# Performance work log

Measured on AMD Instinct MI355X. Metric: run time of the kernel, lower is better.

Reference implementation:

```python
import jax, jax.numpy as jnp
import numpy as np

N = 50000   # nnodes
E = 1600000 # edges (avg degree 32)
F = 128     # nfeatures
D = 64      # output_dim
T = 10      # s2v iterations (default in n2v)


def setup_inputs() -> dict:
    key = jax.random.key(0)
    k_x, k_s, k_d, k_w1, k_w2 = jax.random.split(key, 5)
    x = jax.random.normal(k_x, (N, F), dtype=jnp.float32)
    edge_src = jax.random.randint(k_s, (E,), 0, N, dtype=jnp.int32)
    edge_dst = jax.random.randint(k_d, (E,), 0, N, dtype=jnp.int32)
    # xavier_uniform init as in reset_parameters
    s1 = float(np.sqrt(6.0 / (F + D)))
    s2 = float(np.sqrt(6.0 / (D + D)))
    W1 = jax.random.uniform(k_w1, (D, F), jnp.float32, -s1, s1)
    W2 = jax.random.uniform(k_w2, (D, D), jnp.float32, -s2, s2)
    b1 = jnp.zeros((D,), jnp.float32)
    b2 = jnp.zeros((D,), jnp.float32)
    return {"x": x, "W1": W1, "b1": b1, "W2": W2, "b2": b2,
            "edge_src": edge_src, "edge_dst": edge_dst}


def reference(x, W1, b1, W2, b2, edge_src, edge_dst):
    Wx = x @ W1.T + b1                      # [N, D]

    def step(emb, _):
        # sum of neighbor embeddings: gather sources, segment-sum into dests
        agg = jax.ops.segment_sum(emb[edge_src], edge_dst, num_segments=N)  # [N, D]
        emb_new = jax.nn.relu(Wx + agg @ W2.T + b2)
        return emb_new, None

    emb0 = jnp.zeros((N, D), dtype=x.dtype)
    emb, _ = jax.lax.scan(step, emb0, None, length=T)  # n2v
    # g2v: sum node embeddings into graph embedding
    return emb.sum(axis=0)                  # [D]
```

## Files before the change

### kernel.cpp

```cpp
#include <hip/hip_runtime.h>

#define D 64
#define F 128
#define NBMAX 256
#define DB 128

typedef unsigned int uint;
typedef unsigned short ushort;
typedef short s16x8 __attribute__((ext_vector_type(8)));
typedef float f32x4 __attribute__((ext_vector_type(4)));

__device__ __forceinline__ float bf16lo(uint u) { return __uint_as_float(u << 16); }
__device__ __forceinline__ float bf16hi(uint u) { return __uint_as_float(u & 0xFFFF0000u); }
__device__ __forceinline__ ushort f2bf16(float f) {
    uint u = __float_as_uint(f);
    u += 0x7FFFu + ((u >> 16) & 1u);
    return (ushort)(u >> 16);
}
__device__ __forceinline__ uint pk2bf(float lo, float hi) {
    return (uint)f2bf16(lo) | ((uint)f2bf16(hi) << 16);
}


__global__ __launch_bounds__(256) void bucket_hist(const int* __restrict__ dst,
                                                   int* __restrict__ gb, int E, int nb) {
    __shared__ int h[NBMAX];
    for (int t = threadIdx.x; t < nb; t += 256) h[t] = 0;
    __syncthreads();
    int start = blockIdx.x * 4096;
    int end   = start + 4096 < E ? start + 4096 : E;
    for (int i = start + threadIdx.x; i < end; i += 256)
        atomicAdd(&h[dst[i] >> 8], 1);
    __syncthreads();
    for (int t = threadIdx.x; t < nb; t += 256)
        if (h[t]) atomicAdd(&gb[t], h[t]);
}

__global__ void bucket_scan(const int* __restrict__ gb, int* __restrict__ gboff,
                            int* __restrict__ gcur, int nb) {
    if (threadIdx.x == 0) {
        int s = 0;
        for (int b = 0; b < nb; ++b) { gboff[b] = s; gcur[b] = s; s += gb[b]; }
        gboff[nb] = s;
    }
}

__global__ __launch_bounds__(256) void bucket_scatter(const int* __restrict__ src,
                                                      const int* __restrict__ dst,
                                                      int* __restrict__ gcur,
                                                      int* __restrict__ packed, int E, int nb) {
    __shared__ int h[NBMAX], base[NBMAX], lcur[NBMAX];
    for (int t = threadIdx.x; t < nb; t += 256) h[t] = 0;
    __syncthreads();
    int start = blockIdx.x * 4096;
    int end   = start + 4096 < E ? start + 4096 : E;
    for (int i = start + threadIdx.x; i < end; i += 256)
        atomicAdd(&h[dst[i] >> 8], 1);
    __syncthreads();
    for (int t = threadIdx.x; t < nb; t += 256) {
        base[t] = h[t] ? atomicAdd(&gcur[t], h[t]) : 0;
        lcur[t] = 0;
    }
    __syncthreads();
    for (int i = start + threadIdx.x; i < end; i += 256) {
        int d = dst[i];
        int b = d >> 8;
        int pos = base[b] + atomicAdd(&lcur[b], 1);
        packed[pos] = (src[i] << 8) | (d & 255);
    }
}

__global__ __launch_bounds__(256) void bucket_deg(const int* __restrict__ gboff,
                                                  const int* __restrict__ packed,
                                                  int* __restrict__ deg, int N) {
    __shared__ int h[NBMAX];
    int b = blockIdx.x;
    h[threadIdx.x] = 0;
    __syncthreads();
    int st = gboff[b], en = gboff[b + 1];
    for (int i = st + threadIdx.x; i < en; i += 256)
        atomicAdd(&h[packed[i] & 255], 1);
    __syncthreads();
    int node = (b << 8) + threadIdx.x;
    if (node < N) deg[node] = h[threadIdx.x];
}

__global__ __launch_bounds__(256) void bucket_fill(const int* __restrict__ gboff,
                                                   const int* __restrict__ packed,
                                                   const int* __restrict__ row_ptr,
                                                   const int* __restrict__ rank,
                                                   int* __restrict__ col, int N) {
    __shared__ int lcur[NBMAX];
    int b = blockIdx.x;
    int node = (b << 8) + threadIdx.x;
    lcur[threadIdx.x] = (node < N) ? row_ptr[node] : 0;
    __syncthreads();
    int st = gboff[b], en = gboff[b + 1];
    for (int i = st + threadIdx.x; i < en; i += 256) {
        int p = packed[i];
        int pos = atomicAdd(&lcur[p & 255], 1);
        col[pos] = rank[p >> 8];
    }
}


__global__ void count_deg_kernel(const int* __restrict__ dst, int* __restrict__ deg, int E) {
    int i = blockIdx.x * blockDim.x + threadIdx.x;
    if (i < E) atomicAdd(&deg[dst[i]], 1);
}

__global__ void fill_kernel(const int* __restrict__ src, const int* __restrict__ dst,
                            int* __restrict__ cursor, const int* __restrict__ rank,
                            int* __restrict__ col, int E) {
    int i = blockIdx.x * blockDim.x + threadIdx.x;
    if (i < E) {
        int d_ = dst[i];
        int pos = atomicAdd(&cursor[d_], 1);
        col[pos] = rank[src[i]];
    }
}


__global__ __launch_bounds__(256) void dsort_hist(const int* __restrict__ deg,
                                                  int* __restrict__ dh, int N) {
    __shared__ int h[DB];
    if (threadIdx.x < DB) h[threadIdx.x] = 0;
    __syncthreads();
    int start = blockIdx.x * 4096;
    int end   = start + 4096 < N ? start + 4096 : N;
    for (int i = start + threadIdx.x; i < end; i += 256) {
        int d = deg[i];
        atomicAdd(&h[d < DB - 1 ? d : DB - 1], 1);
    }
    __syncthreads();
    if (threadIdx.x < DB && h[threadIdx.x]) atomicAdd(&dh[threadIdx.x], h[threadIdx.x]);
}

__global__ void dsort_scan(const int* __restrict__ dh, int* __restrict__ dcur) {
    if (threadIdx.x == 0) {
        int s = 0;
        for (int b = 0; b < DB; ++b) { dcur[b] = s; s += dh[b]; }
    }
}

__global__ __launch_bounds__(256) void dsort_scatter(const int* __restrict__ deg,
                                                     int* __restrict__ dcur,
                                                     int* __restrict__ perm,
                                                     int* __restrict__ rank, int N) {
    __shared__ int h[DB], base[DB], lc[DB];
    if (threadIdx.x < DB) h[threadIdx.x] = 0;
    __syncthreads();
    int start = blockIdx.x * 4096;
    int end   = start + 4096 < N ? start + 4096 : N;
    for (int i = start + threadIdx.x; i < end; i += 256) {
        int d = deg[i];
        atomicAdd(&h[d < DB - 1 ? d : DB - 1], 1);
    }
    __syncthreads();
    if (threadIdx.x < DB) {
        base[threadIdx.x] = h[threadIdx.x] ? atomicAdd(&dcur[threadIdx.x], h[threadIdx.x]) : 0;
        lc[threadIdx.x] = 0;
    }
    __syncthreads();
    for (int i = start + threadIdx.x; i < end; i += 256) {
        int d = deg[i];
        int b = d < DB - 1 ? d : DB - 1;
        int pos = base[b] + atomicAdd(&lc[b], 1);
        perm[pos] = i;
        rank[i] = pos;
    }
}


__global__ __launch_bounds__(1024) void scan_kernel(const int* __restrict__ deg,
                                                    int* __restrict__ row_ptr, int n) {
    __shared__ int wsum[16];
    int lane = threadIdx.x & 63;
    int wid  = threadIdx.x >> 6;
    int carry = 0;
    const int CH = 4096;
    for (int base = 0; base < n; base += CH) {
        int i0 = base + (int)threadIdx.x * 4;
        int v0 = (i0     < n) ? deg[i0]     : 0;
        int v1 = (i0 + 1 < n) ? deg[i0 + 1] : 0;
        int v2 = (i0 + 2 < n) ? deg[i0 + 2] : 0;
        int v3 = (i0 + 3 < n) ? deg[i0 + 3] : 0;
        int p0 = v0, p1 = p0 + v1, p2 = p1 + v2, p3 = p2 + v3;
        int tsum = p3;
        int s = tsum;
        #pragma unroll
        for (int off = 1; off < 64; off <<= 1) {
            int t = __shfl_up(s, off);
            if (lane >= off) s += t;
        }
        if (lane == 63) wsum[wid] = s;
        __syncthreads();
        int wbase = 0, chunk_total = 0;
        #pragma unroll
        for (int w = 0; w < 16; ++w) {
            int t = wsum[w];
            chunk_total += t;
            if (w < wid) wbase += t;
        }
        __syncthreads();
        int ex = carry + wbase + (s - tsum);
        if (i0     < n) row_ptr[i0 + 1] = ex + p0;
        if (i0 + 1 < n) row_ptr[i0 + 2] = ex + p1;
        if (i0 + 2 < n) row_ptr[i0 + 3] = ex + p2;
        if (i0 + 3 < n) row_ptr[i0 + 4] = ex + p3;
        carry += chunk_total;
    }
    if (threadIdx.x == 0) row_ptr[0] = 0;
}


__global__ __launch_bounds__(256) void wx_mfma_kernel(const float* __restrict__ x,
                                                      const float* __restrict__ W1,
                                                      const float* __restrict__ b1,
                                                      const float* __restrict__ b2,
                                                      const int* __restrict__ perm,
                                                      float* __restrict__ Wx,
                                                      ushort* __restrict__ emb, int N) {
    int lane = threadIdx.x & 63;
    int wv = blockIdx.x * 4 + (threadIdx.x >> 6);
    int nwaves = gridDim.x * 4;
    int r16 = lane & 15;
    int kg  = lane >> 4;

    s16x8 bf[4][4];
    #pragma unroll
    for (int nt = 0; nt < 4; ++nt) {
        const float* wrow = W1 + (size_t)(nt * 16 + r16) * F;
        #pragma unroll
        for (int ks = 0; ks < 4; ++ks) {
            const float4* p = reinterpret_cast<const float4*>(wrow + ks * 32 + kg * 8);
            float4 f0 = p[0], f1 = p[1];
            union { s16x8 v; uint u[4]; } t;
            t.u[0] = pk2bf(f0.x, f0.y); t.u[1] = pk2bf(f0.z, f0.w);
            t.u[2] = pk2bf(f1.x, f1.y); t.u[3] = pk2bf(f1.z, f1.w);
            bf[nt][ks] = t.v;
        }
    }
    float b1v[4], b2v[4];
    #pragma unroll
    for (int nt = 0; nt < 4; ++nt) {
        b1v[nt] = b1[nt * 16 + r16];
        b2v[nt] = b2[nt * 16 + r16];
    }

    int ntiles = (N + 15) >> 4;
    for (int tile = wv; tile < ntiles; tile += nwaves) {
        int row0 = tile << 4;
        int arow = row0 + r16;
        if (arow >= N) arow = N - 1;
        int orig = perm[arow];
        s16x8 af[4];
        #pragma unroll
        for (int ks = 0; ks < 4; ++ks) {
            const float4* p = reinterpret_cast<const float4*>(x + (size_t)orig * F + ks * 32 + kg * 8);
            float4 f0 = p[0], f1 = p[1];
            union { s16x8 v; uint u[4]; } t;
            t.u[0] = pk2bf(f0.x, f0.y); t.u[1] = pk2bf(f0.z, f0.w);
            t.u[2] = pk2bf(f1.x, f1.y); t.u[3] = pk2bf(f1.z, f1.w);
            af[ks] = t.v;
        }
        #pragma unroll
        for (int nt = 0; nt < 4; ++nt) {
            f32x4 acc = {0.f, 0.f, 0.f, 0.f};
            #pragma unroll
            for (int ks = 0; ks < 4; ++ks)
                acc = __builtin_amdgcn_mfma_f32_16x16x32_bf16(af[ks], bf[nt][ks], acc, 0, 0, 0);
            int outd = nt * 16 + r16;
            #pragma unroll
            for (int r = 0; r < 4; ++r) {
                int node = row0 + kg * 4 + r;
                if (node < N) {
                    float wxv = acc[r] + b1v[nt];
                    Wx[(size_t)node * D + outd] = wxv;
                    float e = wxv + b2v[nt];
                    emb[(size_t)node * D + outd] = f2bf16(e > 0.f ? e : 0.f);
                }
            }
        }
    }
}


__global__ __launch_bounds__(256) void step_kernel(const ushort* __restrict__ emb_in,
                                                   ushort* __restrict__ emb_out,
                                                   const float* __restrict__ Wx,
                                                   const float* __restrict__ W2,
                                                   const float* __restrict__ b2,
                                                   const int* __restrict__ row_ptr,
                                                   const int* __restrict__ col,
                                                   const int* __restrict__ perm, int N) {
    int lane = threadIdx.x & 63;
    int w = threadIdx.x >> 6;
    int r = lane & 15;
    int a = lane >> 4;

    int ntiles = (N + 15) >> 4;
    int tile = ntiles - 1 - (blockIdx.x * 4 + w);
    if (tile < 0) return;

    int rg = tile * 16 + r;
    int rgc = rg < N ? rg : N - 1;
    int node = perm[rgc];
    int rp = row_ptr[node];
    int degr = row_ptr[node + 1] - rp;
    if (rg >= N) degr = 0;
    int maxd = degr;
    #pragma unroll
    for (int off = 1; off < 16; off <<= 1) {
        int o = __shfl_xor(maxd, off);
        maxd = o > maxd ? o : maxd;
    }

    float acc0[8] = {0.f, 0.f, 0.f, 0.f, 0.f, 0.f, 0.f, 0.f};
    float acc1[8] = {0.f, 0.f, 0.f, 0.f, 0.f, 0.f, 0.f, 0.f};

    const ushort* base0 = emb_in + (a << 3);
    const ushort* base1 = emb_in + 32 + (a << 3);

    if (maxd > 0) {
        uint4 c0[4], c1[4];
        #pragma unroll
        for (int j = 0; j < 4; ++j) {
            int u = (j < degr) ? col[rp + j] : N;
            c0[j] = *reinterpret_cast<const uint4*>(base0 + ((size_t)u << 6));
            c1[j] = *reinterpret_cast<const uint4*>(base1 + ((size_t)u << 6));
        }
        int nch = (maxd + 3) >> 2;
        for (int c = 0; c < nch; ++c) {
            uint4 n0[4], n1[4];
            int kb = (c + 1) << 2;
            if (c + 1 < nch) {
                #pragma unroll
                for (int j = 0; j < 4; ++j) {
                    int u = (kb + j < degr) ? col[rp + kb + j] : N;
                    n0[j] = *reinterpret_cast<const uint4*>(base0 + ((size_t)u << 6));
                    n1[j] = *reinterpret_cast<const uint4*>(base1 + ((size_t)u << 6));
                }
            }
            #pragma unroll
            for (int j = 0; j < 4; ++j) {
                acc0[0] += bf16lo(c0[j].x); acc0[1] += bf16hi(c0[j].x);
                acc0[2] += bf16lo(c0[j].y); acc0[3] += bf16hi(c0[j].y);
                acc0[4] += bf16lo(c0[j].z); acc0[5] += bf16hi(c0[j].z);
                acc0[6] += bf16lo(c0[j].w); acc0[7] += bf16hi(c0[j].w);
                acc1[0] += bf16lo(c1[j].x); acc1[1] += bf16hi(c1[j].x);
                acc1[2] += bf16lo(c1[j].y); acc1[3] += bf16hi(c1[j].y);
                acc1[4] += bf16lo(c1[j].z); acc1[5] += bf16hi(c1[j].z);
                acc1[6] += bf16lo(c1[j].w); acc1[7] += bf16hi(c1[j].w);
            }
            #pragma unroll
            for (int j = 0; j < 4; ++j) { c0[j] = n0[j]; c1[j] = n1[j]; }
        }
    }

    s16x8 af[4][2];
    #pragma unroll
    for (int t = 0; t < 4; ++t)
        #pragma unroll
        for (int f = 0; f < 2; ++f) {
            const float4* p = reinterpret_cast<const float4*>(W2 + (size_t)(t * 16 + r) * D + f * 32 + a * 8);
            float4 f0 = p[0], f1 = p[1];
            union { s16x8 v; uint u[4]; } tt;
            tt.u[0] = pk2bf(f0.x, f0.y); tt.u[1] = pk2bf(f0.z, f0.w);
            tt.u[2] = pk2bf(f1.x, f1.y); tt.u[3] = pk2bf(f1.z, f1.w);
            af[t][f] = tt.v;
        }
    float4 b2v[4];
    #pragma unroll
    for (int t = 0; t < 4; ++t)
        b2v[t] = *reinterpret_cast<const float4*>(b2 + t * 16 + a * 4);

    union { s16x8 v; uint u[4]; } B0, B1;
    B0.u[0] = pk2bf(acc0[0], acc0[1]); B0.u[1] = pk2bf(acc0[2], acc0[3]);
    B0.u[2] = pk2bf(acc0[4], acc0[5]); B0.u[3] = pk2bf(acc0[6], acc0[7]);
    B1.u[0] = pk2bf(acc1[0], acc1[1]); B1.u[1] = pk2bf(acc1[2], acc1[3]);
    B1.u[2] = pk2bf(acc1[4], acc1[5]); B1.u[3] = pk2bf(acc1[6], acc1[7]);

    f32x4 d0 = {0.f, 0.f, 0.f, 0.f}, d1 = {0.f, 0.f, 0.f, 0.f};
    f32x4 d2 = {0.f, 0.f, 0.f, 0.f}, d3 = {0.f, 0.f, 0.f, 0.f};
    d0 = __builtin_amdgcn_mfma_f32_16x16x32_bf16(af[0][0], B0.v, d0, 0, 0, 0);
    d1 = __builtin_amdgcn_mfma_f32_16x16x32_bf16(af[1][0], B0.v, d1, 0, 0, 0);
    d2 = __builtin_amdgcn_mfma_f32_16x16x32_bf16(af[2][0], B0.v, d2, 0, 0, 0);
    d3 = __builtin_amdgcn_mfma_f32_16x16x32_bf16(af[3][0], B0.v, d3, 0, 0, 0);
    d0 = __builtin_amdgcn_mfma_f32_16x16x32_bf16(af[0][1], B1.v, d0, 0, 0, 0);
    d1 = __builtin_amdgcn_mfma_f32_16x16x32_bf16(af[1][1], B1.v, d1, 0, 0, 0);
    d2 = __builtin_amdgcn_mfma_f32_16x16x32_bf16(af[2][1], B1.v, d2, 0, 0, 0);
    d3 = __builtin_amdgcn_mfma_f32_16x16x32_bf16(af[3][1], B1.v, d3, 0, 0, 0);

    if (rg < N) {
        const float* wxp = Wx + ((size_t)rg << 6);
        ushort* op = emb_out + ((size_t)rg << 6);
        #pragma unroll
        for (int t = 0; t < 4; ++t) {
            float4 wx4 = *reinterpret_cast<const float4*>(wxp + t * 16 + a * 4);
            f32x4 dd = (t == 0) ? d0 : (t == 1) ? d1 : (t == 2) ? d2 : d3;
            float e0 = wx4.x + b2v[t].x + dd[0];
            float e1 = wx4.y + b2v[t].y + dd[1];
            float e2 = wx4.z + b2v[t].z + dd[2];
            float e3 = wx4.w + b2v[t].w + dd[3];
            e0 = e0 > 0.f ? e0 : 0.f; e1 = e1 > 0.f ? e1 : 0.f;
            e2 = e2 > 0.f ? e2 : 0.f; e3 = e3 > 0.f ? e3 : 0.f;
            uint2 st;
            st.x = pk2bf(e0, e1);
            st.y = pk2bf(e2, e3);
            *reinterpret_cast<uint2*>(op + t * 16 + a * 4) = st;
        }
    }
}


__global__ __launch_bounds__(256) void reduce_kernel(const ushort* __restrict__ emb,
                                                     float* __restrict__ out, int N) {
    int lane = threadIdx.x & 63;
    int wid  = threadIdx.x >> 6;
    float acc = 0.f;
    int nw = gridDim.x * 4;
    for (int v = blockIdx.x * 4 + wid; v < N; v += nw)
        acc += __uint_as_float((uint)emb[(size_t)v * D + lane] << 16);
    __shared__ float red[256];
    red[threadIdx.x] = acc;
    __syncthreads();
    if (threadIdx.x < 64) {
        float sum = red[threadIdx.x] + red[threadIdx.x + 64] +
                    red[threadIdx.x + 128] + red[threadIdx.x + 192];
        atomicAdd(&out[threadIdx.x], sum);
    }
}

extern "C" void kernel_launch(void* const* d_in, const int* in_sizes, int n_in,
                              void* d_out, int out_size, void* d_ws, size_t ws_size,
                              hipStream_t stream) {
    const float* x    = (const float*)d_in[0];
    const float* W1   = (const float*)d_in[1];
    const float* b1   = (const float*)d_in[2];
    const float* W2   = (const float*)d_in[3];
    const float* b2   = (const float*)d_in[4];
    const int*   esrc = (const int*)d_in[5];
    const int*   edst = (const int*)d_in[6];
    int N = in_sizes[0] / F;
    int E = in_sizes[5];
    float* out = (float*)d_out;

    char* ws = (char*)d_ws;
    size_t off = 0;
    auto alloc = [&](size_t bytes) -> char* {
        char* p = ws + off;
        off += (bytes + 255) & ~(size_t)255;
        return p;
    };
    float*  Wx      = (float*)alloc((size_t)N * D * 4);
    ushort* embA    = (ushort*)alloc(((size_t)N + 1) * D * 2);
    ushort* embB    = (ushort*)alloc(((size_t)N + 1) * D * 2);
    int*    row_ptr = (int*)alloc(((size_t)N + 1) * 4);
    int*    deg     = (int*)alloc((size_t)N * 4);
    int*    col     = (int*)alloc((size_t)E * 4);
    int*    packed  = (int*)alloc((size_t)E * 4);
    int*    perm    = (int*)alloc(((size_t)N + 16) * 4);
    int*    rank    = (int*)alloc((size_t)N * 4);
    int*    gb      = (int*)alloc((NBMAX + 1) * 4);
    int*    gboff   = (int*)alloc((NBMAX + 1) * 4);
    int*    gcur    = (int*)alloc((NBMAX + 1) * 4);
    int*    dh      = (int*)alloc(DB * 4);
    int*    dcur    = (int*)alloc(DB * 4);
    int*    cursor  = (int*)alloc((size_t)N * 4);

    hipMemsetAsync(out, 0, (size_t)out_size * 4, stream);
    hipMemsetAsync(embA + (size_t)N * D, 0, D * 2, stream);
    hipMemsetAsync(embB + (size_t)N * D, 0, D * 2, stream);
    hipMemsetAsync(dh, 0, DB * 4, stream);

    int nb = ((N - 1) >> 8) + 1;
    int nchunksE = (E + 4095) / 4096;
    int nchunksN = (N + 4095) / 4096;
    if (N <= 65536) {
        hipMemsetAsync(gb, 0, (size_t)nb * 4, stream);
        bucket_hist<<<nchunksE, 256, 0, stream>>>(edst, gb, E, nb);
        bucket_scan<<<1, 64, 0, stream>>>(gb, gboff, gcur, nb);
        bucket_scatter<<<nchunksE, 256, 0, stream>>>(esrc, edst, gcur, packed, E, nb);
        bucket_deg<<<nb, 256, 0, stream>>>(gboff, packed, deg, N);
        dsort_hist<<<nchunksN, 256, 0, stream>>>(deg, dh, N);
        dsort_scan<<<1, 64, 0, stream>>>(dh, dcur);
        dsort_scatter<<<nchunksN, 256, 0, stream>>>(deg, dcur, perm, rank, N);
        scan_kernel<<<1, 1024, 0, stream>>>(deg, row_ptr, N);
        bucket_fill<<<nb, 256, 0, stream>>>(gboff, packed, row_ptr, rank, col, N);
    } else {
        hipMemsetAsync(deg, 0, (size_t)N * 4, stream);
        count_deg_kernel<<<(E + 255) / 256, 256, 0, stream>>>(edst, deg, E);
        dsort_hist<<<nchunksN, 256, 0, stream>>>(deg, dh, N);
        dsort_scan<<<1, 64, 0, stream>>>(dh, dcur);
        dsort_scatter<<<nchunksN, 256, 0, stream>>>(deg, dcur, perm, rank, N);
        scan_kernel<<<1, 1024, 0, stream>>>(deg, row_ptr, N);
        hipMemcpyAsync(cursor, row_ptr, (size_t)N * 4, hipMemcpyDeviceToDevice, stream);
        fill_kernel<<<(E + 255) / 256, 256, 0, stream>>>(esrc, edst, cursor, rank, col, E);
    }

    wx_mfma_kernel<<<256, 256, 0, stream>>>(x, W1, b1, b2, perm, Wx, embA, N);

    int ntiles = (N + 15) >> 4;
    int sblocks = (ntiles + 3) / 4;
    ushort* pin = embA;
    ushort* pout = embB;
    for (int t = 1; t < 10; ++t) {
        step_kernel<<<sblocks, 256, 0, stream>>>(pin, pout, Wx, W2, b2, row_ptr, col, perm, N);
        ushort* tmp = pin; pin = pout; pout = tmp;
    }
    reduce_kernel<<<256, 256, 0, stream>>>(pin, out, N);
}
```

Before: 589.4 us.

## Split each 16-node tile's neighbor gather across four waves with LDS reduction

Each step block now handles one 16-row tile instead of four. The four waves each gather a quarter of the neighbors (interleaved in groups of 4), and waves 1-3 write their partial sums to shared memory. Wave 0 then reduces them and runs the MFMA/epilogue. This is meant to cut per-wave serial latency for high-degree rows and to expose more memory-level parallelism. The cost is four times as many blocks, a __syncthreads, LDS traffic, and three waves sitting idle during the matmul phase.

```diff
diff --git a/kernel.cpp b/kernel.cpp
--- a/kernel.cpp
+++ b/kernel.cpp
@@ -294,14 +294,13 @@
                                                    const int* __restrict__ row_ptr,
                                                    const int* __restrict__ col,
                                                    const int* __restrict__ perm, int N) {
+    __shared__ float part[3][16][64];
     int lane = threadIdx.x & 63;
     int w = threadIdx.x >> 6;
     int r = lane & 15;
     int a = lane >> 4;
 
-    int ntiles = (N + 15) >> 4;
-    int tile = ntiles - 1 - (blockIdx.x * 4 + w);
-    if (tile < 0) return;
+    int tile = (int)(gridDim.x - 1 - blockIdx.x);
 
     int rg = tile * 16 + r;
     int rgc = rg < N ? rg : N - 1;
@@ -322,22 +321,24 @@
     const ushort* base0 = emb_in + (a << 3);
     const ushort* base1 = emb_in + 32 + (a << 3);
 
-    if (maxd > 0) {
+    int nch = (maxd + 15) >> 4;
+    if (nch > 0) {
         uint4 c0[4], c1[4];
         #pragma unroll
         for (int j = 0; j < 4; ++j) {
-            int u = (j < degr) ? col[rp + j] : N;
+            int idx = (w << 2) + j;
+            int u = (idx < degr) ? col[rp + idx] : N;
             c0[j] = *reinterpret_cast<const uint4*>(base0 + ((size_t)u << 6));
             c1[j] = *reinterpret_cast<const uint4*>(base1 + ((size_t)u << 6));
         }
-        int nch = (maxd + 3) >> 2;
         for (int c = 0; c < nch; ++c) {
             uint4 n0[4], n1[4];
-            int kb = (c + 1) << 2;
+            int kb = ((c + 1) << 4) + (w << 2);
             if (c + 1 < nch) {
                 #pragma unroll
                 for (int j = 0; j < 4; ++j) {
-                    int u = (kb + j < degr) ? col[rp + kb + j] : N;
+                    int idx = kb + j;
+                    int u = (idx < degr) ? col[rp + idx] : N;
                     n0[j] = *reinterpret_cast<const uint4*>(base0 + ((size_t)u << 6));
                     n1[j] = *reinterpret_cast<const uint4*>(base1 + ((size_t)u << 6));
                 }
@@ -356,6 +357,21 @@
             #pragma unroll
             for (int j = 0; j < 4; ++j) { c0[j] = n0[j]; c1[j] = n1[j]; }
         }
+    }
+
+    if (w > 0) {
+        #pragma unroll
+        for (int j = 0; j < 8; ++j) {
+            part[w - 1][j][lane]     = acc0[j];
+            part[w - 1][8 + j][lane] = acc1[j];
+        }
+    }
+    __syncthreads();
+    if (w != 0) return;
+    #pragma unroll
+    for (int j = 0; j < 8; ++j) {
+        acc0[j] += part[0][j][lane] + part[1][j][lane] + part[2][j][lane];
+        acc1[j] += part[0][8 + j][lane] + part[1][8 + j][lane] + part[2][8 + j][lane];
     }
 
     s16x8 af[4][2];
@@ -502,11 +518,10 @@
     wx_mfma_kernel<<<256, 256, 0, stream>>>(x, W1, b1, b2, perm, Wx, embA, N);
 
     int ntiles = (N + 15) >> 4;
-    int sblocks = (ntiles + 3) / 4;
     ushort* pin = embA;
     ushort* pout = embB;
     for (int t = 1; t < 10; ++t) {
-        step_kernel<<<sblocks, 256, 0, stream>>>(pin, pout, Wx, W2, b2, row_ptr, col, perm, N);
+        step_kernel<<<ntiles, 256, 0, stream>>>(pin, pout, Wx, W2, b2, row_ptr, col, perm, N);
         ushort* tmp = pin; pin = pout; pout = tmp;
     }
     reduce_kernel<<<256, 256, 0, stream>>>(pin, out, N);
```

Result: no change. 593.1 us (+0.6%).
